# Optimization experiments

Hardware: AMD Instinct MI355X
Metric: run time of the kernel (lower is better)

## Reference

```python
import jax, jax.numpy as jnp
import numpy as np


def _dwconv3d(x, w, b):
    # depthwise Conv3d, kernel 3, stride 1, padding 1 (SAME), groups = channels
    groups = x.shape[1]
    y = jax.lax.conv_general_dilated(
        x, w, window_strides=(1, 1, 1), padding='SAME',
        feature_group_count=groups,
        dimension_numbers=('NCDHW', 'OIDHW', 'NCDHW'))
    return y + b[None, :, None, None, None]


def setup_inputs() -> dict:
    key = jax.random.key(0)
    ks = jax.random.split(key, 8)
    B, C, K, D, H, W = 4, 64, 64, 16, 64, 64
    sc = 0.1
    return {
        'x_q': jax.random.normal(ks[0], (B, C, D, H, W), jnp.float32),
        'x_kv': jax.random.normal(ks[1], (B, K, D, H, W), jnp.float32),
        'wq': jax.random.normal(ks[2], (C, 1, 3, 3, 3), jnp.float32) * sc,
        'bq': jax.random.normal(ks[3], (C,), jnp.float32) * sc,
        'wk': jax.random.normal(ks[4], (K, 1, 3, 3, 3), jnp.float32) * sc,
        'bk': jax.random.normal(ks[5], (K,), jnp.float32) * sc,
        'wv': jax.random.normal(ks[6], (K, 1, 3, 3, 3), jnp.float32) * sc,
        'bv': jax.random.normal(ks[7], (K,), jnp.float32) * sc,
    }


def reference(x_q, x_kv, wq, bq, wk, bk, wv, bv):
    q = _dwconv3d(x_q, wq, bq)   # [B,C,D,H,W]
    k = _dwconv3d(x_kv, wk, bk)  # [B,K,D,H,W]
    v = _dwconv3d(x_kv, wv, bv)  # [B,K,D,H,W]
    B, C = q.shape[:2]
    K = k.shape[1]
    qf = q.reshape(B, C, -1)     # [B,C,S]
    kf = k.reshape(B, K, -1)     # [B,K,S]
    vf = v.reshape(B, K, -1)     # [B,K,S]
    attn = jnp.einsum('bcs,bks->bck', qf, kf) / jnp.sqrt(jnp.asarray(K, qf.dtype))
    attn = jax.nn.softmax(attn, axis=-1)           # [B,C,K]
    n = int(0.1 * C)
    at = attn.transpose(0, 2, 1)                   # [B,K,C]
    _, idx = jax.lax.top_k(at, n)                  # [B,K,n] indices into C
    mask = jnp.sum(jax.nn.one_hot(idx, C, dtype=attn.dtype), axis=-2)  # [B,K,C]
    attn_m = attn * mask.transpose(0, 2, 1)        # [B,C,K], NOT renormalized
    out = jnp.einsum('bck,bks->bcs', attn_m, vf).reshape(q.shape)
    return x_q + out, attn_m
```

## Files before the change

kernel.cpp:

```cpp
#include <hip/hip_runtime.h>
#include <math.h>

#define BB   4
#define CC   64
#define KK   64
#define DDim 16
#define HDim 64
#define WDim 64
#define SS   (DDim*HDim*WDim)
#define PLANE (HDim*WDim)
#define NCH2 64
#define TOPN 6

typedef __attribute__((ext_vector_type(8))) short bf16x8;
typedef __attribute__((ext_vector_type(4))) float f32x4;

__device__ __forceinline__ unsigned cvt_pk_bf16(float lo, float hi) {
    unsigned r;
    asm("v_cvt_pk_bf16_f32 %0, %1, %2" : "=v"(r) : "v"(lo), "v"(hi));
    return r;
}
__device__ __forceinline__ float bf2f(unsigned short u) {
    union { unsigned u; float f; } v; v.u = ((unsigned)u) << 16; return v.f;
}

__global__ __launch_bounds__(128) void conv_reg(
    const float* __restrict__ xq, const float* __restrict__ xkv,
    const float* __restrict__ wq, const float* __restrict__ bq,
    const float* __restrict__ wk, const float* __restrict__ bk,
    const float* __restrict__ wv, const float* __restrict__ bv,
    unsigned short* __restrict__ qo, unsigned short* __restrict__ ko,
    unsigned short* __restrict__ vo)
{
    int bid  = blockIdx.x;
    int work = (bid & 7) * 256 + (bid >> 3);
    int t  = work >> 10;
    int b  = (work >> 8) & 3;
    int c  = (work >> 2) & 63;
    int hs = work & 3;
    int g0 = hs << 4;

    const float* src = (t ? xkv : xq) + (size_t)(b*CC + c) * SS;
    float wA[27], wB[27], bA, bB;
    if (t == 0) {
        #pragma unroll
        for (int i = 0; i < 27; ++i) { wA[i] = wq[c*27 + i]; wB[i] = 0.f; }
        bA = bq[c]; bB = 0.f;
    } else {
        #pragma unroll
        for (int i = 0; i < 27; ++i) { wA[i] = wk[c*27 + i]; wB[i] = wv[c*27 + i]; }
        bA = bk[c]; bB = bv[c];
    }
    unsigned short* dA = (t ? ko : qo) + (size_t)(b*CC + c) * SS;
    unsigned short* dB = vo + (size_t)(b*CC + c) * SS;

    const int tid  = threadIdx.x;
    const int lane = tid & 63;
    const int wg   = tid & 7;
    const int w0   = wg << 3;
    const int hl   = tid >> 3;
    const int y    = g0 + hl;

    float4 stg[3][2];
    float  W0[3][10], W1[3][10], W2[3][10];

#define GLOAD(p) {                                                             \
    _Pragma("unroll")                                                          \
    for (int rr_ = 0; rr_ < 3; ++rr_) {                                        \
        const int gy_ = y - 1 + rr_;                                           \
        float4 a0_ = make_float4(0.f,0.f,0.f,0.f), a1_ = a0_;                  \
        if ((p) < DDim && gy_ >= 0 && gy_ < HDim) {                            \
            const float* bp_ = src + (size_t)(p)*PLANE + gy_*WDim + w0;        \
            a0_ = *(const float4*)(bp_);                                       \
            a1_ = *(const float4*)(bp_ + 4);                                   \
        }                                                                      \
        stg[rr_][0] = a0_; stg[rr_][1] = a1_;                                  \
    } }

#define CONSUME(W) {                                                           \
    _Pragma("unroll")                                                          \
    for (int rr_ = 0; rr_ < 3; ++rr_) {                                        \
        float lh_ = __shfl(stg[rr_][1].w, lane - 1, 64);                       \
        float rh_ = __shfl(stg[rr_][0].x, lane + 1, 64);                       \
        W[rr_][0] = wg       ? lh_ : 0.f;                                      \
        W[rr_][9] = (wg < 7) ? rh_ : 0.f;                                      \
        W[rr_][1]=stg[rr_][0].x; W[rr_][2]=stg[rr_][0].y;                      \
        W[rr_][3]=stg[rr_][0].z; W[rr_][4]=stg[rr_][0].w;                      \
        W[rr_][5]=stg[rr_][1].x; W[rr_][6]=stg[rr_][1].y;                      \
        W[rr_][7]=stg[rr_][1].z; W[rr_][8]=stg[rr_][1].w;                      \
    } }

#define FMAS(W, dz, DOB) {                                                     \
    _Pragma("unroll")                                                          \
    for (int dy_ = 0; dy_ < 3; ++dy_) {                                        \
        const float ca0_ = wA[(dz)*9 + dy_*3 + 0];                             \
        const float ca1_ = wA[(dz)*9 + dy_*3 + 1];                             \
        const float ca2_ = wA[(dz)*9 + dy_*3 + 2];                             \
        const float cb0_ = wB[(dz)*9 + dy_*3 + 0];                             \
        const float cb1_ = wB[(dz)*9 + dy_*3 + 1];                             \
        const float cb2_ = wB[(dz)*9 + dy_*3 + 2];                             \
        _Pragma("unroll")                                                      \
        for (int j_ = 0; j_ < 8; ++j_) {                                       \
            float sA_ = fmaf(ca0_, W[dy_][j_],   accA[j_]);                    \
            sA_       = fmaf(ca1_, W[dy_][j_+1], sA_);                         \
            accA[j_]  = fmaf(ca2_, W[dy_][j_+2], sA_);                         \
            if (DOB) {                                                         \
                float sB_ = fmaf(cb0_, W[dy_][j_],   accB[j_]);                \
                sB_       = fmaf(cb1_, W[dy_][j_+1], sB_);                     \
                accB[j_]  = fmaf(cb2_, W[dy_][j_+2], sB_);                     \
            }                                                                  \
        }                                                                      \
    } }

#define STEP(dd, Wa, Wb, Wc, DOB) {                                            \
    CONSUME(Wc);                        \
    GLOAD((dd)+2);                       \
    float accA[8], accB[8];                                                    \
    _Pragma("unroll")                                                          \
    for (int j_ = 0; j_ < 8; ++j_) { accA[j_] = bA; accB[j_] = bB; }           \
    FMAS(Wa, 0, DOB);                                                          \
    FMAS(Wb, 1, DOB);                                                          \
    FMAS(Wc, 2, DOB);                                                          \
    const int off_ = (dd)*PLANE + y*WDim + w0;                                 \
    uint4 pkA_;                                                                \
    pkA_.x = cvt_pk_bf16(accA[0], accA[1]);                                    \
    pkA_.y = cvt_pk_bf16(accA[2], accA[3]);                                    \
    pkA_.z = cvt_pk_bf16(accA[4], accA[5]);                                    \
    pkA_.w = cvt_pk_bf16(accA[6], accA[7]);                                    \
    *(uint4*)&dA[off_] = pkA_;                                                 \
    if (DOB) {                                                                 \
        uint4 pkB_;                                                            \
        pkB_.x = cvt_pk_bf16(accB[0], accB[1]);                                \
        pkB_.y = cvt_pk_bf16(accB[2], accB[3]);                                \
        pkB_.z = cvt_pk_bf16(accB[4], accB[5]);                                \
        pkB_.w = cvt_pk_bf16(accB[6], accB[7]);                                \
        *(uint4*)&dB[off_] = pkB_;                                             \
    } }

    #pragma unroll
    for (int rr = 0; rr < 3; ++rr)
        #pragma unroll
        for (int j = 0; j < 10; ++j) W2[rr][j] = 0.f;
    GLOAD(0); CONSUME(W0);
    GLOAD(1);

#define STEP3(dbase, DOB)                                                      \
    STEP(dbase,     W2, W0, W1, DOB);                                          \
    STEP((dbase)+1, W0, W1, W2, DOB);                                          \
    STEP((dbase)+2, W1, W2, W0, DOB);

    if (t == 0) {
        STEP3(0, 0) STEP3(3, 0) STEP3(6, 0) STEP3(9, 0) STEP3(12, 0)
        STEP(15, W2, W0, W1, 0);
    } else {
        STEP3(0, 1) STEP3(3, 1) STEP3(6, 1) STEP3(9, 1) STEP3(12, 1)
        STEP(15, W2, W0, W1, 1);
    }
#undef GLOAD
#undef CONSUME
#undef FMAS
#undef STEP
#undef STEP3
}

__global__ __launch_bounds__(256) void gemm1_mfma(
    const unsigned short* __restrict__ qb, const unsigned short* __restrict__ kb,
    float* __restrict__ part)
{
    __shared__ unsigned short lq[64*136];
    __shared__ unsigned short lk[64*136];

    int bid   = blockIdx.x;
    int b     = bid >> 6;
    int chunk = bid & 63;
    int tid   = threadIdx.x;
    int lane  = tid & 63;
    int wid   = tid >> 6;
    int c0    = wid << 4;
    int lr    = lane & 15;
    int kq    = lane >> 4;

    const unsigned short* qsrc = qb + (size_t)b*CC*SS;
    const unsigned short* ksrc = kb + (size_t)b*KK*SS;

    f32x4 acc[4];
    #pragma unroll
    for (int j = 0; j < 4; ++j) acc[j] = (f32x4){0.f, 0.f, 0.f, 0.f};

    const int sbase = chunk << 10;
    for (int sc = 0; sc < 8; ++sc) {
        const int s0 = sbase + (sc << 7);
        __syncthreads();
        #pragma unroll
        for (int it = 0; it < 8; ++it) {
            const int idx  = it*256 + tid;
            const int tile = idx >> 10;
            const int row  = (idx >> 4) & 63;
            const int ch8  = idx & 15;
            const unsigned short* s_ = (tile ? ksrc : qsrc) + (size_t)row*SS + s0 + ch8*8;
            unsigned short* d_ = (tile ? lk : lq) + row*136 + ch8*8;
            *(uint4*)d_ = *(const uint4*)s_;
        }
        __syncthreads();
        #pragma unroll
        for (int ss = 0; ss < 4; ++ss) {
            const int scol = ss*32 + kq*8;
            bf16x8 a = *(const bf16x8*)&lq[(c0 + lr)*136 + scol];
            #pragma unroll
            for (int j = 0; j < 4; ++j) {
                bf16x8 bv = *(const bf16x8*)&lk[(j*16 + lr)*136 + scol];
                acc[j] = __builtin_amdgcn_mfma_f32_16x16x32_bf16(a, bv, acc[j], 0, 0, 0);
            }
        }
    }

    float* pb = part + ((size_t)(b*NCH2 + chunk)) * (CC*KK);
    #pragma unroll
    for (int j = 0; j < 4; ++j)
        #pragma unroll
        for (int r = 0; r < 4; ++r)
            pb[(c0 + kq*4 + r)*KK + j*16 + lr] = acc[j][r];
}

__global__ __launch_bounds__(256) void reduce_attn(
    const float* __restrict__ part, float* __restrict__ attn)
{
    int bid = blockIdx.x;
    int b = bid >> 6, c = bid & 63;
    int tid = threadIdx.x;
    int k = tid & 63, g = tid >> 6;
    float s = 0.f;
    for (int ch = g; ch < NCH2; ch += 4)
        s += part[(size_t)(b*NCH2 + ch)*(CC*KK) + c*KK + k];
    __shared__ float red[256];
    red[tid] = s;
    __syncthreads();
    if (tid < 64) {
        float tot = red[tid] + red[tid+64] + red[tid+128] + red[tid+192];
        attn[b*CC*KK + c*KK + tid] = tot * 0.125f;
    }
}

__global__ __launch_bounds__(64) void softmax_topk(
    const float* __restrict__ attn, float* __restrict__ attn_m)
{
    __shared__ float p[64*65];
    int b = blockIdx.x;
    int t = threadIdx.x;
    for (int i = 0; i < 64; ++i) p[i*65 + t] = attn[b*4096 + i*64 + t];
    __syncthreads();
    float m = -1e30f;
    for (int k = 0; k < 64; ++k) m = fmaxf(m, p[t*65 + k]);
    float sum = 0.f;
    for (int k = 0; k < 64; ++k) { float e = expf(p[t*65+k] - m); p[t*65+k] = e; sum += e; }
    float inv = 1.f / sum;
    for (int k = 0; k < 64; ++k) p[t*65+k] *= inv;
    __syncthreads();
    unsigned long long chosen = 0ull;
    #pragma unroll
    for (int pass = 0; pass < TOPN; ++pass) {
        float best = -1.f; int bi = 0;
        for (int c2 = 0; c2 < 64; ++c2) {
            float v = p[c2*65 + t];
            if (!((chosen >> c2) & 1ull) && v > best) { best = v; bi = c2; }
        }
        chosen |= 1ull << bi;
    }
    for (int c2 = 0; c2 < 64; ++c2) {
        float v = p[c2*65 + t];
        attn_m[b*4096 + c2*64 + t] = ((chosen >> c2) & 1ull) ? v : 0.f;
    }
}

__global__ __launch_bounds__(256) void gemm2_out(
    const float* __restrict__ attn_m, const unsigned short* __restrict__ v,
    const float* __restrict__ xq, float* __restrict__ out)
{
    __shared__ float amt[64][68];
    __shared__ float vt[64][132];
    int bid = blockIdx.x;
    int b  = bid >> 7;
    int ch = bid & 127;
    int tid = threadIdx.x;
    for (int i = 0; i < 16; ++i) {
        int idx = i*256 + tid;
        amt[idx & 63][idx >> 6] = attn_m[b*4096 + idx];
    }
    int c0 = (tid >> 4) * 4;
    int s0 = (tid & 15) * 8;
    const unsigned short* vb = v + (size_t)b*KK*SS;
    const float* xb = xq + (size_t)b*CC*SS;
    float* ob = out + (size_t)b*CC*SS;
    int sb0 = ch * 512;
    for (int st = 0; st < 4; ++st) {
        int sb = sb0 + st*128;
        __syncthreads();
        #pragma unroll
        for (int i = 0; i < 4; ++i) {
            int idx = i*256 + tid;
            int k   = idx >> 4;
            int s8  = (idx & 15) * 8;
            uint4 pk = *(const uint4*)&vb[(size_t)k*SS + sb + s8];
            float* dst = &vt[k][s8];
            dst[0] = bf2f((unsigned short)(pk.x & 0xffff));
            dst[1] = bf2f((unsigned short)(pk.x >> 16));
            dst[2] = bf2f((unsigned short)(pk.y & 0xffff));
            dst[3] = bf2f((unsigned short)(pk.y >> 16));
            dst[4] = bf2f((unsigned short)(pk.z & 0xffff));
            dst[5] = bf2f((unsigned short)(pk.z >> 16));
            dst[6] = bf2f((unsigned short)(pk.w & 0xffff));
            dst[7] = bf2f((unsigned short)(pk.w >> 16));
        }
        __syncthreads();
        float acc[4][8] = {};
        #pragma unroll 8
        for (int k = 0; k < 64; ++k) {
            float4 a  = *(const float4*)&amt[k][c0];
            float4 v0 = *(const float4*)&vt[k][s0];
            float4 v1 = *(const float4*)&vt[k][s0+4];
            float av[4] = {a.x,a.y,a.z,a.w};
            float vv[8] = {v0.x,v0.y,v0.z,v0.w,v1.x,v1.y,v1.z,v1.w};
            #pragma unroll
            for (int i = 0; i < 4; ++i)
                #pragma unroll
                for (int j = 0; j < 8; ++j)
                    acc[i][j] = fmaf(av[i], vv[j], acc[i][j]);
        }
        #pragma unroll
        for (int i = 0; i < 4; ++i) {
            int off = (c0+i)*SS + sb + s0;
            float4 x0 = *(const float4*)&xb[off];
            float4 x1 = *(const float4*)&xb[off+4];
            *(float4*)&ob[off]   = make_float4(acc[i][0]+x0.x, acc[i][1]+x0.y,
                                               acc[i][2]+x0.z, acc[i][3]+x0.w);
            *(float4*)&ob[off+4] = make_float4(acc[i][4]+x1.x, acc[i][5]+x1.y,
                                               acc[i][6]+x1.z, acc[i][7]+x1.w);
        }
    }
}

extern "C" void kernel_launch(void* const* d_in, const int* in_sizes, int n_in,
                              void* d_out, int out_size, void* d_ws, size_t ws_size,
                              hipStream_t stream)
{
    const float* xq  = (const float*)d_in[0];
    const float* xkv = (const float*)d_in[1];
    const float* wq  = (const float*)d_in[2];
    const float* bq  = (const float*)d_in[3];
    const float* wk  = (const float*)d_in[4];
    const float* bk  = (const float*)d_in[5];
    const float* wv  = (const float*)d_in[6];
    const float* bv  = (const float*)d_in[7];
    float* out = (float*)d_out;

    unsigned short* k_ws = (unsigned short*)d_ws;
    unsigned short* v_ws = k_ws + (size_t)BB*KK*SS;
    float* part = (float*)(v_ws + (size_t)BB*KK*SS);
    float* attn = part + (size_t)BB*NCH2*CC*KK;

    unsigned short* q_bf = (unsigned short*)out;
    float* attn_m = out + (size_t)BB*CC*SS;

    conv_reg   <<<2*BB*CC*4, 128, 0, stream>>>(xq, xkv, wq, bq, wk, bk, wv, bv,
                                               q_bf, k_ws, v_ws);
    gemm1_mfma <<<BB*NCH2,   256, 0, stream>>>(q_bf, k_ws, part);
    reduce_attn<<<BB*CC,     256, 0, stream>>>(part, attn);
    softmax_topk<<<BB,        64, 0, stream>>>(attn, attn_m);
    gemm2_out  <<<BB*128,    256, 0, stream>>>(attn_m, v_ws, xq, out);
}
```

Measured before the change: 147.3 us.

## Stage conv input planes through LDS ring buffer with larger tiles

The depthwise conv kernel now uses 256-thread blocks that each cover 32 rows instead of 16. Each depth plane (34 rows with halo) is loaded once cooperatively into a three-slot shared-memory ring, and each thread reads its three rows from there instead of loading all three from global memory. This removes the threefold redundant global loads of overlapping rows and halves the halo overhead. In exchange it adds a __syncthreads per depth step and uses about 27KB of LDS per block, which may limit occupancy.

```diff
diff --git a/kernel.cpp b/kernel.cpp
--- a/kernel.cpp
+++ b/kernel.cpp
@@ -11,6 +11,7 @@
 #define PLANE (HDim*WDim)
 #define NCH2 64
 #define TOPN 6
+#define RSTR 68
 
 typedef __attribute__((ext_vector_type(8))) short bf16x8;
 typedef __attribute__((ext_vector_type(4))) float f32x4;
@@ -24,7 +25,7 @@
     union { unsigned u; float f; } v; v.u = ((unsigned)u) << 16; return v.f;
 }
 
-__global__ __launch_bounds__(128) void conv_reg(
+__global__ __launch_bounds__(256) void conv_hyb(
     const float* __restrict__ xq, const float* __restrict__ xkv,
     const float* __restrict__ wq, const float* __restrict__ bq,
     const float* __restrict__ wk, const float* __restrict__ bk,
@@ -32,13 +33,15 @@
     unsigned short* __restrict__ qo, unsigned short* __restrict__ ko,
     unsigned short* __restrict__ vo)
 {
+    __shared__ float ring[3][34*RSTR];
+
     int bid  = blockIdx.x;
-    int work = (bid & 7) * 256 + (bid >> 3);
-    int t  = work >> 10;
-    int b  = (work >> 8) & 3;
-    int c  = (work >> 2) & 63;
-    int hs = work & 3;
-    int g0 = hs << 4;
+    int work = (bid & 7) * 128 + (bid >> 3);
+    int t  = work >> 9;
+    int b  = (work >> 7) & 3;
+    int c  = (work >> 1) & 63;
+    int hh = work & 1;
+    int g0 = hh << 5;
 
     const float* src = (t ? xkv : xq) + (size_t)(b*CC + c) * SS;
     float wA[27], wB[27], bA, bB;
@@ -61,33 +64,63 @@
     const int hl   = tid >> 3;
     const int y    = g0 + hl;
 
-    float4 stg[3][2];
+    float4 stg[3];
     float  W0[3][10], W1[3][10], W2[3][10];
 
-#define GLOAD(p) {                                                             \
+#define SLOAD(p) {                                                             \
+    const int p_ = (p);                                                        \
+    const bool pv_ = (p_ >= 0 && p_ < DDim);                                   \
+    _Pragma("unroll")                                                          \
+    for (int i_ = 0; i_ < 3; ++i_) {                                           \
+        const int fidx_ = i_*256 + tid;                                        \
+        const int row_  = fidx_ >> 4;                                          \
+        const int gy_   = g0 - 1 + row_;                                       \
+        float4 v_ = make_float4(0.f,0.f,0.f,0.f);                              \
+        if (pv_ && fidx_ < 544 && gy_ >= 0 && gy_ < HDim)                      \
+            v_ = *(const float4*)(src + (size_t)p_*PLANE + gy_*WDim            \
+                                  + (fidx_ & 15)*4);                           \
+        stg[i_] = v_;                                                          \
+    } }
+#define SWRITE(slot) {                                                         \
+    float* R_ = ring[slot];                                                    \
+    _Pragma("unroll")                                                          \
+    for (int i_ = 0; i_ < 3; ++i_) {                                           \
+        const int fidx_ = i_*256 + tid;                                        \
+        if (fidx_ < 544)                                                       \
+            *(float4*)&R_[(fidx_ >> 4)*RSTR + (fidx_ & 15)*4] = stg[i_];       \
+    } }
+
+#define LREAD(W, slot) {                                                       \
+    const float* R_ = ring[slot];                                              \
+    _Pragma("unroll")                                                          \
+    for (int rr_ = 0; rr_ < 3; ++rr_) {                                        \
+        const int base_ = (hl + rr_)*RSTR + w0;                                \
+        float4 a0_ = *(const float4*)&R_[base_];                               \
+        float4 a1_ = *(const float4*)&R_[base_ + 4];                           \
+        float lh_ = __shfl(a1_.w, lane - 1, 64);                               \
+        float rh_ = __shfl(a0_.x, lane + 1, 64);                               \
+        W[rr_][0] = wg       ? lh_ : 0.f;                                      \
+        W[rr_][9] = (wg < 7) ? rh_ : 0.f;                                      \
+        W[rr_][1]=a0_.x; W[rr_][2]=a0_.y; W[rr_][3]=a0_.z; W[rr_][4]=a0_.w;    \
+        W[rr_][5]=a1_.x; W[rr_][6]=a1_.y; W[rr_][7]=a1_.z; W[rr_][8]=a1_.w;    \
+    } }
+
+#define GREAD0(W) {                                                            \
     _Pragma("unroll")                                                          \
     for (int rr_ = 0; rr_ < 3; ++rr_) {                                        \
         const int gy_ = y - 1 + rr_;                                           \
         float4 a0_ = make_float4(0.f,0.f,0.f,0.f), a1_ = a0_;                  \
-        if ((p) < DDim && gy_ >= 0 && gy_ < HDim) {                            \
-            const float* bp_ = src + (size_t)(p)*PLANE + gy_*WDim + w0;        \
+        if (gy_ >= 0 && gy_ < HDim) {                                          \
+            const float* bp_ = src + gy_*WDim + w0;                            \
             a0_ = *(const float4*)(bp_);                                       \
             a1_ = *(const float4*)(bp_ + 4);                                   \
         }                                                                      \
-        stg[rr_][0] = a0_; stg[rr_][1] = a1_;                                  \
-    } }
-
-#define CONSUME(W) {                                                           \
-    _Pragma("unroll")                                                          \
-    for (int rr_ = 0; rr_ < 3; ++rr_) {                                        \
-        float lh_ = __shfl(stg[rr_][1].w, lane - 1, 64);                       \
-        float rh_ = __shfl(stg[rr_][0].x, lane + 1, 64);                       \
+        float lh_ = __shfl(a1_.w, lane - 1, 64);                               \
+        float rh_ = __shfl(a0_.x, lane + 1, 64);                               \
         W[rr_][0] = wg       ? lh_ : 0.f;                                      \
         W[rr_][9] = (wg < 7) ? rh_ : 0.f;                                      \
-        W[rr_][1]=stg[rr_][0].x; W[rr_][2]=stg[rr_][0].y;                      \
-        W[rr_][3]=stg[rr_][0].z; W[rr_][4]=stg[rr_][0].w;                      \
-        W[rr_][5]=stg[rr_][1].x; W[rr_][6]=stg[rr_][1].y;                      \
-        W[rr_][7]=stg[rr_][1].z; W[rr_][8]=stg[rr_][1].w;                      \
+        W[rr_][1]=a0_.x; W[rr_][2]=a0_.y; W[rr_][3]=a0_.z; W[rr_][4]=a0_.w;    \
+        W[rr_][5]=a1_.x; W[rr_][6]=a1_.y; W[rr_][7]=a1_.z; W[rr_][8]=a1_.w;    \
     } }
 
 #define FMAS(W, dz, DOB) {                                                     \
@@ -112,9 +145,9 @@
         }                                                                      \
     } }
 
-#define STEP(dd, Wa, Wb, Wc, DOB) {                                            \
-    CONSUME(Wc);                        \
-    GLOAD((dd)+2);                       \
+#define STEP(dd, Wa, Wb, Wc, RS, WS, DOB) {                                    \
+    LREAD(Wc, RS);                                   \
+    if ((dd) < 15) SLOAD((dd) + 2);             \
     float accA[8], accB[8];                                                    \
     _Pragma("unroll")                                                          \
     for (int j_ = 0; j_ < 8; ++j_) { accA[j_] = bA; accB[j_] = bB; }           \
@@ -135,29 +168,34 @@
         pkB_.z = cvt_pk_bf16(accB[4], accB[5]);                                \
         pkB_.w = cvt_pk_bf16(accB[6], accB[7]);                                \
         *(uint4*)&dB[off_] = pkB_;                                             \
-    } }
+    }                                                                          \
+    if ((dd) < 15) { SWRITE(WS); __syncthreads(); }                            \
+    }
 
     #pragma unroll
     for (int rr = 0; rr < 3; ++rr)
         #pragma unroll
         for (int j = 0; j < 10; ++j) W2[rr][j] = 0.f;
-    GLOAD(0); CONSUME(W0);
-    GLOAD(1);
+    GREAD0(W0);
+    SLOAD(1); SWRITE(1);
+    __syncthreads();
 
 #define STEP3(dbase, DOB)                                                      \
-    STEP(dbase,     W2, W0, W1, DOB);                                          \
-    STEP((dbase)+1, W0, W1, W2, DOB);                                          \
-    STEP((dbase)+2, W1, W2, W0, DOB);
+    STEP(dbase,     W2, W0, W1, 1, 2, DOB);                                    \
+    STEP((dbase)+1, W0, W1, W2, 2, 0, DOB);                                    \
+    STEP((dbase)+2, W1, W2, W0, 0, 1, DOB);
 
     if (t == 0) {
         STEP3(0, 0) STEP3(3, 0) STEP3(6, 0) STEP3(9, 0) STEP3(12, 0)
-        STEP(15, W2, W0, W1, 0);
+        STEP(15, W2, W0, W1, 1, 2, 0);
     } else {
         STEP3(0, 1) STEP3(3, 1) STEP3(6, 1) STEP3(9, 1) STEP3(12, 1)
-        STEP(15, W2, W0, W1, 1);
-    }
-#undef GLOAD
-#undef CONSUME
+        STEP(15, W2, W0, W1, 1, 2, 1);
+    }
+#undef SLOAD
+#undef SWRITE
+#undef LREAD
+#undef GREAD0
 #undef FMAS
 #undef STEP
 #undef STEP3
@@ -361,7 +399,7 @@
     unsigned short* q_bf = (unsigned short*)out;
     float* attn_m = out + (size_t)BB*CC*SS;
 
-    conv_reg   <<<2*BB*CC*4, 128, 0, stream>>>(xq, xkv, wq, bq, wk, bk, wv, bv,
+    conv_hyb   <<<2*BB*CC*2, 256, 0, stream>>>(xq, xkv, wq, bq, wk, bk, wv, bv,
                                                q_bf, k_ws, v_ws);
     gemm1_mfma <<<BB*NCH2,   256, 0, stream>>>(q_bf, k_ws, part);
     reduce_attn<<<BB*CC,     256, 0, stream>>>(part, attn);
```

New measurement: 166.2 us. 1.13x slower.
